# Kernel optimization log

Hardware: AMD Instinct MI355X
Metric: run time of the kernel (lower is better)

The kernel has to match this reference:

```python
import jax, jax.numpy as jnp
import numpy as np

T, J, D = 8192, 1024, 256  # context len, query len, 2*hidden


def setup_inputs() -> dict:
    key = jax.random.key(0)
    k1, k2, k3 = jax.random.split(key, 3)
    context = jax.random.normal(k1, (T, D), dtype=jnp.float32)
    query = jax.random.normal(k2, (J, D), dtype=jnp.float32)
    # sim_weight: Linear(3*D, 1, bias=False) -> single weight vector of length 3*D
    w = jax.random.normal(k3, (3 * D,), dtype=jnp.float32) * (1.0 / np.sqrt(3 * D))
    return {"context": context, "query": query, "w": w}


def reference(context, query, w):
    D = context.shape[1]
    # Decompose w.[c; q; c*q] into three rank-1 / matmul terms instead of
    # materializing [T,J,3D] concatenated pairs.
    w_c, w_q, w_m = w[:D], w[D:2 * D], w[2 * D:]
    # S[t,j] = c_t.w_c + q_j.w_q + (c_t * w_m).q_j   -> [T, J]
    S = (context @ w_c)[:, None] + (query @ w_q)[None, :] + (context * w_m) @ query.T
    # context-to-query attention: softmax over query positions j
    A = jax.nn.softmax(S, axis=1)                    # [T, J]
    context2query = A @ query                        # [T, D]
    # NOTE: original code takes b = max_j S (no softmax over t) and
    # h_tilde = sum_t b[t] * c_t  (a single [D] vector)
    b = jnp.max(S, axis=1)                           # [T]
    h_tilde = b @ context                            # [D]
    # G[t] = [c_t; c2q_t; c_t*c2q_t; c_t*h_tilde]    -> [T, 4D]
    G = jnp.concatenate(
        [context, context2query, context * context2query, context * h_tilde[None, :]],
        axis=1,
    )
    return G
```

## Files before the change

### kernel.cpp

```cpp
#include <hip/hip_runtime.h>
#include <stdint.h>

#define T_DIM 8192
#define J_DIM 1024
#define D_DIM 256

typedef __bf16 bf16x8 __attribute__((ext_vector_type(8)));
typedef float f32x4 __attribute__((ext_vector_type(4)));
typedef unsigned short u16x8 __attribute__((ext_vector_type(8)));
typedef unsigned short u16x4 __attribute__((ext_vector_type(4)));

__device__ inline unsigned short f2bf(float x) {
    unsigned u = __builtin_bit_cast(unsigned, x);
    u += 0x7FFFu + ((u >> 16) & 1u);
    return (unsigned short)(u >> 16);
}

__device__ inline void gll16(const void* g, void* l) {
    __builtin_amdgcn_global_load_lds(
        (const __attribute__((address_space(1))) unsigned int*)g,
        (__attribute__((address_space(3))) unsigned int*)l, 16, 0, 0);
}

__global__ __launch_bounds__(256) void prep_all(const float* __restrict__ ctx,
                                                const float* __restrict__ qry,
                                                const float* __restrict__ w,
                                                unsigned short* __restrict__ Cm,
                                                float* __restrict__ cw,
                                                unsigned short* __restrict__ Qb,
                                                unsigned short* __restrict__ QT,
                                                float* __restrict__ qw,
                                                float* __restrict__ stats) {
    int wid = threadIdx.x >> 6, lane = threadIdx.x & 63;
    if (blockIdx.x >= 2304) {
        int idx = (blockIdx.x - 2304) * 256 + threadIdx.x;
        if (idx < 2 * T_DIM + D_DIM) stats[idx] = 0.0f;
        return;
    }
    if (blockIdx.x < 2048) {
        int t = blockIdx.x * 4 + wid;
        float4 c  = *(const float4*)(ctx + (size_t)t * D_DIM + lane * 4);
        float4 wm = *(const float4*)(w + 2 * D_DIM + lane * 4);
        float4 wc = *(const float4*)(w + lane * 4);
        u16x4 cmv;
        cmv[0] = f2bf(c.x * wm.x);
        cmv[1] = f2bf(c.y * wm.y);
        cmv[2] = f2bf(c.z * wm.z);
        cmv[3] = f2bf(c.w * wm.w);
        *(u16x4*)(Cm + (size_t)t * D_DIM + lane * 4) = cmv;
        float s = c.x * wc.x + c.y * wc.y + c.z * wc.z + c.w * wc.w;
        #pragma unroll
        for (int o = 1; o < 64; o <<= 1) s += __shfl_xor(s, o);
        if (lane == 0) cw[t] = s;
    } else {
        int j = (blockIdx.x - 2048) * 4 + wid;
        float4 c  = *(const float4*)(qry + (size_t)j * D_DIM + lane * 4);
        float4 wq = *(const float4*)(w + D_DIM + lane * 4);
        u16x4 qv;
        qv[0] = f2bf(c.x);
        qv[1] = f2bf(c.y);
        qv[2] = f2bf(c.z);
        qv[3] = f2bf(c.w);
        *(u16x4*)(Qb + (size_t)j * D_DIM + lane * 4) = qv;
        int d0 = lane * 4;
        QT[(size_t)(d0 + 0) * J_DIM + j] = qv[0];
        QT[(size_t)(d0 + 1) * J_DIM + j] = qv[1];
        QT[(size_t)(d0 + 2) * J_DIM + j] = qv[2];
        QT[(size_t)(d0 + 3) * J_DIM + j] = qv[3];
        float s = c.x * wq.x + c.y * wq.y + c.z * wq.z + c.w * wq.w;
        #pragma unroll
        for (int o = 1; o < 64; o <<= 1) s += __shfl_xor(s, o);
        if (lane == 0) qw[j] = s;
    }
}

__global__ __launch_bounds__(256) void gemm_s(const unsigned short* __restrict__ Cm,
                                              const unsigned short* __restrict__ Qb,
                                              const float* __restrict__ qw,
                                              unsigned short* __restrict__ P,
                                              float* __restrict__ lsum,
                                              int* __restrict__ rmax) {
    __shared__ unsigned short SH[12288];
    __shared__ float statS[2][64];
    __shared__ float statM[2][64];
    unsigned short* As = SH;
    unsigned short* Bs = SH + 4096;
    int tid = threadIdx.x, lane = tid & 63, wv = tid >> 6;
    int wm = wv >> 1, wn = wv & 1;
    int bm = blockIdx.x & 127, bn = blockIdx.x >> 7;
    int cidx = lane & 15, rgrp = lane >> 4;
    int srow8 = lane >> 3;
    int swzc = (lane & 7) ^ srow8;
    f32x4 acc[2][4] = {};

    const unsigned short* Asrc = Cm + (size_t)(bm * 64 + srow8) * 256 + (swzc << 3);
    const unsigned short* Bsrc = Qb + (size_t)(bn * 128 + srow8) * 256 + (swzc << 3);

    for (int k0 = 0; k0 < 256; k0 += 64) {
        if (k0) __syncthreads();
        #pragma unroll
        for (int i = 0; i < 2; ++i) {
            int g = wv * 2 + i;
            gll16(Asrc + (size_t)(g * 8) * 256 + k0, As + g * 512);
        }
        #pragma unroll
        for (int i = 0; i < 4; ++i) {
            int g = wv * 4 + i;
            gll16(Bsrc + (size_t)(g * 8) * 256 + k0, Bs + g * 512);
        }
        __syncthreads();
        #pragma unroll
        for (int ks = 0; ks < 2; ++ks) {
            int klo = ks * 4 + rgrp;
            bf16x8 af[2], bfr[4];
            #pragma unroll
            for (int m = 0; m < 2; ++m) {
                int ra = wm * 32 + m * 16 + cidx;
                af[m] = __builtin_bit_cast(bf16x8,
                        *(const u16x8*)(As + ra * 64 + ((klo ^ (ra & 7)) << 3)));
            }
            #pragma unroll
            for (int n = 0; n < 4; ++n) {
                int rb = wn * 64 + n * 16 + cidx;
                bfr[n] = __builtin_bit_cast(bf16x8,
                        *(const u16x8*)(Bs + rb * 64 + ((klo ^ (rb & 7)) << 3)));
            }
            #pragma unroll
            for (int m = 0; m < 2; ++m)
                #pragma unroll
                for (int n = 0; n < 4; ++n)
                    acc[m][n] = __builtin_amdgcn_mfma_f32_16x16x32_bf16(af[m], bfr[n], acc[m][n], 0, 0, 0);
        }
    }

    float qwv[4];
    #pragma unroll
    for (int n = 0; n < 4; ++n) qwv[n] = qw[bn * 128 + wn * 64 + n * 16 + cidx];
    #pragma unroll
    for (int m = 0; m < 2; ++m) {
        #pragma unroll
        for (int rg = 0; rg < 4; ++rg) {
            float s = 0.f, mx = 0.f;
            #pragma unroll
            for (int n = 0; n < 4; ++n) {
                float p = __expf(acc[m][n][rg] + qwv[n]);
                acc[m][n][rg] = p;
                s += p;
                mx = fmaxf(mx, p);
            }
            #pragma unroll
            for (int o = 1; o < 16; o <<= 1) {
                s += __shfl_xor(s, o);
                mx = fmaxf(mx, __shfl_xor(mx, o));
            }
            if (cidx == 0) {
                int row = wm * 32 + m * 16 + rgrp * 4 + rg;
                statS[wn][row] = s;
                statM[wn][row] = mx;
            }
        }
    }
    __syncthreads();
    if (tid < 64) {
        atomicAdd(lsum + bm * 64 + tid, statS[0][tid] + statS[1][tid]);
        atomicMax(rmax + bm * 64 + tid,
                  __float_as_int(fmaxf(statM[0][tid], statM[1][tid])));
    }

    #pragma unroll
    for (int m = 0; m < 2; ++m)
        #pragma unroll
        for (int n = 0; n < 4; ++n)
            #pragma unroll
            for (int rg = 0; rg < 4; ++rg) {
                int row = wm * 32 + m * 16 + rgrp * 4 + rg;
                int col = wn * 64 + n * 16 + cidx;
                SH[row * 128 + (((col >> 3) ^ (row & 7)) << 3) + (col & 7)] = f2bf(acc[m][n][rg]);
            }
    __syncthreads();
    #pragma unroll
    for (int i = 0; i < 4; ++i) {
        int r = i * 16 + (tid >> 4);
        int c8 = tid & 15;
        u16x8 v = *(const u16x8*)(SH + r * 128 + ((c8 ^ (r & 7)) << 3));
        *(u16x8*)(P + (size_t)(bm * 64 + r) * J_DIM + bn * 128 + c8 * 8) = v;
    }
}

__global__ __launch_bounds__(256) void hb_kernel(const float* __restrict__ rmaxf,
                                                 const float* __restrict__ cw,
                                                 const float* __restrict__ ctx,
                                                 float* __restrict__ ht) {
    __shared__ float bsh[64];
    int tid = threadIdx.x;
    int t0b = blockIdx.x * 64;
    if (tid < 64) bsh[tid] = __logf(rmaxf[t0b + tid]) + cw[t0b + tid];
    __syncthreads();
    float pb = 0.f;
    #pragma unroll 8
    for (int r = 0; r < 64; ++r)
        pb += bsh[r] * ctx[(size_t)(t0b + r) * D_DIM + tid];
    atomicAdd(ht + tid, pb);
}

__global__ __launch_bounds__(256) void gemm_o(const unsigned short* __restrict__ P,
                                              const unsigned short* __restrict__ QT,
                                              const float* __restrict__ lsum,
                                              const float* __restrict__ ht,
                                              const float* __restrict__ ctx,
                                              float* __restrict__ G) {
    __shared__ unsigned short As[4096];
    __shared__ unsigned short Bs[4096];
    int tid = threadIdx.x, lane = tid & 63, wv = tid >> 6;
    int wm = wv >> 1, wn = wv & 1;
    int bm = blockIdx.x & 127, bn = blockIdx.x >> 7;
    int cidx = lane & 15, rgrp = lane >> 4;
    int srow8 = lane >> 3;
    int swzc = (lane & 7) ^ srow8;
    f32x4 acc[2][2] = {};

    const unsigned short* Ap = P  + (size_t)(bm * 64 + srow8) * J_DIM + (swzc << 3);
    const unsigned short* Bp = QT + (size_t)(bn * 64 + srow8) * J_DIM + (swzc << 3);

    for (int k0 = 0; k0 < 1024; k0 += 64) {
        if (k0) __syncthreads();
        #pragma unroll
        for (int i = 0; i < 2; ++i) {
            int g = wv * 2 + i;
            gll16(Ap + (size_t)(g * 8) * J_DIM + k0, As + g * 512);
        }
        #pragma unroll
        for (int i = 0; i < 2; ++i) {
            int g = wv * 2 + i;
            gll16(Bp + (size_t)(g * 8) * J_DIM + k0, Bs + g * 512);
        }
        __syncthreads();
        #pragma unroll
        for (int ks = 0; ks < 2; ++ks) {
            int klo = ks * 4 + rgrp;
            bf16x8 af[2], bfr[2];
            #pragma unroll
            for (int m = 0; m < 2; ++m) {
                int ra = wm * 32 + m * 16 + cidx;
                af[m] = __builtin_bit_cast(bf16x8,
                        *(const u16x8*)(As + ra * 64 + ((klo ^ (ra & 7)) << 3)));
            }
            #pragma unroll
            for (int n = 0; n < 2; ++n) {
                int rb = wn * 32 + n * 16 + cidx;
                bfr[n] = __builtin_bit_cast(bf16x8,
                        *(const u16x8*)(Bs + rb * 64 + ((klo ^ (rb & 7)) << 3)));
            }
            #pragma unroll
            for (int m = 0; m < 2; ++m)
                #pragma unroll
                for (int n = 0; n < 2; ++n)
                    acc[m][n] = __builtin_amdgcn_mfma_f32_16x16x32_bf16(af[m], bfr[n], acc[m][n], 0, 0, 0);
        }
    }

    float htv[2];
    #pragma unroll
    for (int n = 0; n < 2; ++n) htv[n] = ht[bn * 64 + wn * 32 + n * 16 + cidx];
    #pragma unroll
    for (int m = 0; m < 2; ++m) {
        #pragma unroll
        for (int rg = 0; rg < 4; ++rg) {
            int t = bm * 64 + wm * 32 + m * 16 + rgrp * 4 + rg;
            float linv = 1.0f / lsum[t];
            float* gr = G + (size_t)t * 1024;
            #pragma unroll
            for (int n = 0; n < 2; ++n) {
                int d = bn * 64 + wn * 32 + n * 16 + cidx;
                float val = acc[m][n][rg] * linv;
                float c = ctx[(size_t)t * D_DIM + d];
                gr[d]       = c;
                gr[256 + d] = val;
                gr[512 + d] = c * val;
                gr[768 + d] = c * htv[n];
            }
        }
    }
}

extern "C" void kernel_launch(void* const* d_in, const int* in_sizes, int n_in,
                              void* d_out, int out_size, void* d_ws, size_t ws_size,
                              hipStream_t stream) {
    (void)in_sizes; (void)n_in; (void)out_size; (void)ws_size;
    const float* ctx = (const float*)d_in[0];
    const float* qry = (const float*)d_in[1];
    const float* w   = (const float*)d_in[2];
    float* G = (float*)d_out;
    char* ws = (char*)d_ws;

    constexpr size_t OFF_P  = 0;
    constexpr size_t OFF_CM = OFF_P  + (size_t)T_DIM * J_DIM * 2;
    constexpr size_t OFF_QB = OFF_CM + (size_t)T_DIM * D_DIM * 2;
    constexpr size_t OFF_QT = OFF_QB + (size_t)J_DIM * D_DIM * 2;
    constexpr size_t OFF_CW = OFF_QT + (size_t)D_DIM * J_DIM * 2;
    constexpr size_t OFF_QW = OFF_CW + (size_t)T_DIM * 4;
    constexpr size_t OFF_ST = OFF_QW + (size_t)J_DIM * 4;

    unsigned short* P  = (unsigned short*)(ws + OFF_P);
    unsigned short* Cm = (unsigned short*)(ws + OFF_CM);
    unsigned short* Qb = (unsigned short*)(ws + OFF_QB);
    unsigned short* QT = (unsigned short*)(ws + OFF_QT);
    float* cw    = (float*)(ws + OFF_CW);
    float* qw    = (float*)(ws + OFF_QW);
    float* stats = (float*)(ws + OFF_ST);
    float* lsum  = stats;
    float* rmax  = stats + T_DIM;
    float* ht    = stats + 2 * T_DIM;

    prep_all<<<dim3(2369), 256, 0, stream>>>(ctx, qry, w, Cm, cw, Qb, QT, qw, stats);
    gemm_s<<<dim3(1024), 256, 0, stream>>>(Cm, Qb, qw, P, lsum, (int*)rmax);
    hb_kernel<<<dim3(128), 256, 0, stream>>>(rmax, cw, ctx, ht);
    gemm_o<<<dim3(512), 256, 0, stream>>>(P, QT, lsum, ht, ctx, G);
}
```

Measured before the change: 47.28 us.

## Double-buffer LDS tiles in both GEMM kernels to overlap loads with MFMA

Both GEMM kernels switch from a single LDS tile buffer to two buffers. The global-to-LDS load for the next K step is issued before computing on the current one, with an explicit vmcnt wait and barrier at the end of each step. This hides global load latency behind MFMA work and drops one barrier per iteration. The cost is doubled LDS use per block, which may lower occupancy, and gemm_s reuses the B buffer for its output staging.

```diff
diff --git a/kernel.cpp b/kernel.cpp
--- a/kernel.cpp
+++ b/kernel.cpp
@@ -20,6 +20,18 @@
     __builtin_amdgcn_global_load_lds(
         (const __attribute__((address_space(1))) unsigned int*)g,
         (__attribute__((address_space(3))) unsigned int*)l, 16, 0, 0);
+}
+
+__device__ inline void vm0_bar() {
+    asm volatile("s_waitcnt vmcnt(0)" ::: "memory");
+    __builtin_amdgcn_sched_barrier(0);
+    __builtin_amdgcn_s_barrier();
+    __builtin_amdgcn_sched_barrier(0);
+}
+__device__ inline void bar_only() {
+    __builtin_amdgcn_sched_barrier(0);
+    __builtin_amdgcn_s_barrier();
+    __builtin_amdgcn_sched_barrier(0);
 }
 
 __global__ __launch_bounds__(256) void prep_all(const float* __restrict__ ctx,
@@ -80,11 +92,10 @@
                                               unsigned short* __restrict__ P,
                                               float* __restrict__ lsum,
                                               int* __restrict__ rmax) {
-    __shared__ unsigned short SH[12288];
+    __shared__ unsigned short As[2][4096];
+    __shared__ unsigned short Bs[2][8192];
     __shared__ float statS[2][64];
     __shared__ float statM[2][64];
-    unsigned short* As = SH;
-    unsigned short* Bs = SH + 4096;
     int tid = threadIdx.x, lane = tid & 63, wv = tid >> 6;
     int wm = wv >> 1, wn = wv & 1;
     int bm = blockIdx.x & 127, bn = blockIdx.x >> 7;
@@ -96,19 +107,25 @@
     const unsigned short* Asrc = Cm + (size_t)(bm * 64 + srow8) * 256 + (swzc << 3);
     const unsigned short* Bsrc = Qb + (size_t)(bn * 128 + srow8) * 256 + (swzc << 3);
 
-    for (int k0 = 0; k0 < 256; k0 += 64) {
-        if (k0) __syncthreads();
+    auto stage = [&](int buf, int k0) {
         #pragma unroll
         for (int i = 0; i < 2; ++i) {
             int g = wv * 2 + i;
-            gll16(Asrc + (size_t)(g * 8) * 256 + k0, As + g * 512);
+            gll16(Asrc + (size_t)(g * 8) * 256 + k0, &As[buf][g * 512]);
         }
         #pragma unroll
         for (int i = 0; i < 4; ++i) {
             int g = wv * 4 + i;
-            gll16(Bsrc + (size_t)(g * 8) * 256 + k0, Bs + g * 512);
-        }
-        __syncthreads();
+            gll16(Bsrc + (size_t)(g * 8) * 256 + k0, &Bs[buf][g * 512]);
+        }
+    };
+
+    stage(0, 0);
+    vm0_bar();
+    #pragma unroll
+    for (int step = 0; step < 4; ++step) {
+        const int cur = step & 1;
+        if (step < 3) stage(cur ^ 1, (step + 1) * 64);
         #pragma unroll
         for (int ks = 0; ks < 2; ++ks) {
             int klo = ks * 4 + rgrp;
@@ -117,13 +134,13 @@
             for (int m = 0; m < 2; ++m) {
                 int ra = wm * 32 + m * 16 + cidx;
                 af[m] = __builtin_bit_cast(bf16x8,
-                        *(const u16x8*)(As + ra * 64 + ((klo ^ (ra & 7)) << 3)));
+                        *(const u16x8*)(&As[cur][ra * 64 + ((klo ^ (ra & 7)) << 3)]));
             }
             #pragma unroll
             for (int n = 0; n < 4; ++n) {
                 int rb = wn * 64 + n * 16 + cidx;
                 bfr[n] = __builtin_bit_cast(bf16x8,
-                        *(const u16x8*)(Bs + rb * 64 + ((klo ^ (rb & 7)) << 3)));
+                        *(const u16x8*)(&Bs[cur][rb * 64 + ((klo ^ (rb & 7)) << 3)]));
             }
             #pragma unroll
             for (int m = 0; m < 2; ++m)
@@ -131,6 +148,7 @@
                 for (int n = 0; n < 4; ++n)
                     acc[m][n] = __builtin_amdgcn_mfma_f32_16x16x32_bf16(af[m], bfr[n], acc[m][n], 0, 0, 0);
         }
+        if (step < 3) vm0_bar(); else bar_only();
     }
 
     float qwv[4];
@@ -167,6 +185,7 @@
                   __float_as_int(fmaxf(statM[0][tid], statM[1][tid])));
     }
 
+    unsigned short* PT = &Bs[0][0];
     #pragma unroll
     for (int m = 0; m < 2; ++m)
         #pragma unroll
@@ -175,14 +194,14 @@
             for (int rg = 0; rg < 4; ++rg) {
                 int row = wm * 32 + m * 16 + rgrp * 4 + rg;
                 int col = wn * 64 + n * 16 + cidx;
-                SH[row * 128 + (((col >> 3) ^ (row & 7)) << 3) + (col & 7)] = f2bf(acc[m][n][rg]);
+                PT[row * 128 + (((col >> 3) ^ (row & 7)) << 3) + (col & 7)] = f2bf(acc[m][n][rg]);
             }
     __syncthreads();
     #pragma unroll
     for (int i = 0; i < 4; ++i) {
         int r = i * 16 + (tid >> 4);
         int c8 = tid & 15;
-        u16x8 v = *(const u16x8*)(SH + r * 128 + ((c8 ^ (r & 7)) << 3));
+        u16x8 v = *(const u16x8*)(PT + r * 128 + ((c8 ^ (r & 7)) << 3));
         *(u16x8*)(P + (size_t)(bm * 64 + r) * J_DIM + bn * 128 + c8 * 8) = v;
     }
 }
@@ -209,8 +228,8 @@
                                               const float* __restrict__ ht,
                                               const float* __restrict__ ctx,
                                               float* __restrict__ G) {
-    __shared__ unsigned short As[4096];
-    __shared__ unsigned short Bs[4096];
+    __shared__ unsigned short As[2][4096];
+    __shared__ unsigned short Bs[2][4096];
     int tid = threadIdx.x, lane = tid & 63, wv = tid >> 6;
     int wm = wv >> 1, wn = wv & 1;
     int bm = blockIdx.x & 127, bn = blockIdx.x >> 7;
@@ -222,19 +241,21 @@
     const unsigned short* Ap = P  + (size_t)(bm * 64 + srow8) * J_DIM + (swzc << 3);
     const unsigned short* Bp = QT + (size_t)(bn * 64 + srow8) * J_DIM + (swzc << 3);
 
-    for (int k0 = 0; k0 < 1024; k0 += 64) {
-        if (k0) __syncthreads();
+    auto stage = [&](int buf, int k0) {
         #pragma unroll
         for (int i = 0; i < 2; ++i) {
             int g = wv * 2 + i;
-            gll16(Ap + (size_t)(g * 8) * J_DIM + k0, As + g * 512);
-        }
-        #pragma unroll
-        for (int i = 0; i < 2; ++i) {
-            int g = wv * 2 + i;
-            gll16(Bp + (size_t)(g * 8) * J_DIM + k0, Bs + g * 512);
-        }
-        __syncthreads();
+            gll16(Ap + (size_t)(g * 8) * J_DIM + k0, &As[buf][g * 512]);
+            gll16(Bp + (size_t)(g * 8) * J_DIM + k0, &Bs[buf][g * 512]);
+        }
+    };
+
+    stage(0, 0);
+    vm0_bar();
+    #pragma unroll
+    for (int step = 0; step < 16; ++step) {
+        const int cur = step & 1;
+        if (step < 15) stage(cur ^ 1, (step + 1) * 64);
         #pragma unroll
         for (int ks = 0; ks < 2; ++ks) {
             int klo = ks * 4 + rgrp;
@@ -243,13 +264,13 @@
             for (int m = 0; m < 2; ++m) {
                 int ra = wm * 32 + m * 16 + cidx;
                 af[m] = __builtin_bit_cast(bf16x8,
-                        *(const u16x8*)(As + ra * 64 + ((klo ^ (ra & 7)) << 3)));
+                        *(const u16x8*)(&As[cur][ra * 64 + ((klo ^ (ra & 7)) << 3)]));
             }
             #pragma unroll
             for (int n = 0; n < 2; ++n) {
                 int rb = wn * 32 + n * 16 + cidx;
                 bfr[n] = __builtin_bit_cast(bf16x8,
-                        *(const u16x8*)(Bs + rb * 64 + ((klo ^ (rb & 7)) << 3)));
+                        *(const u16x8*)(&Bs[cur][rb * 64 + ((klo ^ (rb & 7)) << 3)]));
             }
             #pragma unroll
             for (int m = 0; m < 2; ++m)
@@ -257,6 +278,7 @@
                 for (int n = 0; n < 2; ++n)
                     acc[m][n] = __builtin_amdgcn_mfma_f32_16x16x32_bf16(af[m], bfr[n], acc[m][n], 0, 0, 0);
         }
+        if (step < 15) vm0_bar(); else bar_only();
     }
 
     float htv[2];
```

Result: slower. 53.12 us (+12.4%).

## Enlarge gemm_s M tile to 128 rows and move c·w_c into hb_kernel

Applied to the files above, without the earlier changes.

The score GEMM now uses 128x128 tiles, giving each wave a 64x64 sub-tile instead of 32x64, which halves the grid to 512 blocks and raises reuse of the query tile loaded into LDS. The context-dot-w_c projection is no longer computed in the prep kernel and stored to workspace. hb_kernel now computes it directly from ctx, with four lanes per row. This removes the cw buffer and a shuffle reduction from prep, but adds register pressure (16 accumulators per wave) and fewer blocks for occupancy in gemm_s.

```diff
diff --git a/kernel.cpp b/kernel.cpp
--- a/kernel.cpp
+++ b/kernel.cpp
@@ -26,7 +26,6 @@
                                                 const float* __restrict__ qry,
                                                 const float* __restrict__ w,
                                                 unsigned short* __restrict__ Cm,
-                                                float* __restrict__ cw,
                                                 unsigned short* __restrict__ Qb,
                                                 unsigned short* __restrict__ QT,
                                                 float* __restrict__ qw,
@@ -41,17 +40,12 @@
         int t = blockIdx.x * 4 + wid;
         float4 c  = *(const float4*)(ctx + (size_t)t * D_DIM + lane * 4);
         float4 wm = *(const float4*)(w + 2 * D_DIM + lane * 4);
-        float4 wc = *(const float4*)(w + lane * 4);
         u16x4 cmv;
         cmv[0] = f2bf(c.x * wm.x);
         cmv[1] = f2bf(c.y * wm.y);
         cmv[2] = f2bf(c.z * wm.z);
         cmv[3] = f2bf(c.w * wm.w);
         *(u16x4*)(Cm + (size_t)t * D_DIM + lane * 4) = cmv;
-        float s = c.x * wc.x + c.y * wc.y + c.z * wc.z + c.w * wc.w;
-        #pragma unroll
-        for (int o = 1; o < 64; o <<= 1) s += __shfl_xor(s, o);
-        if (lane == 0) cw[t] = s;
     } else {
         int j = (blockIdx.x - 2048) * 4 + wid;
         float4 c  = *(const float4*)(qry + (size_t)j * D_DIM + lane * 4);
@@ -80,27 +74,27 @@
                                               unsigned short* __restrict__ P,
                                               float* __restrict__ lsum,
                                               int* __restrict__ rmax) {
-    __shared__ unsigned short SH[12288];
-    __shared__ float statS[2][64];
-    __shared__ float statM[2][64];
+    __shared__ unsigned short SH[16384];
+    __shared__ float statS[2][128];
+    __shared__ float statM[2][128];
     unsigned short* As = SH;
-    unsigned short* Bs = SH + 4096;
+    unsigned short* Bs = SH + 8192;
     int tid = threadIdx.x, lane = tid & 63, wv = tid >> 6;
     int wm = wv >> 1, wn = wv & 1;
-    int bm = blockIdx.x & 127, bn = blockIdx.x >> 7;
+    int bm = blockIdx.x & 63, bn = blockIdx.x >> 6;
     int cidx = lane & 15, rgrp = lane >> 4;
     int srow8 = lane >> 3;
     int swzc = (lane & 7) ^ srow8;
-    f32x4 acc[2][4] = {};
-
-    const unsigned short* Asrc = Cm + (size_t)(bm * 64 + srow8) * 256 + (swzc << 3);
+    f32x4 acc[4][4] = {};
+
+    const unsigned short* Asrc = Cm + (size_t)(bm * 128 + srow8) * 256 + (swzc << 3);
     const unsigned short* Bsrc = Qb + (size_t)(bn * 128 + srow8) * 256 + (swzc << 3);
 
     for (int k0 = 0; k0 < 256; k0 += 64) {
         if (k0) __syncthreads();
         #pragma unroll
-        for (int i = 0; i < 2; ++i) {
-            int g = wv * 2 + i;
+        for (int i = 0; i < 4; ++i) {
+            int g = wv * 4 + i;
             gll16(Asrc + (size_t)(g * 8) * 256 + k0, As + g * 512);
         }
         #pragma unroll
@@ -112,10 +106,10 @@
         #pragma unroll
         for (int ks = 0; ks < 2; ++ks) {
             int klo = ks * 4 + rgrp;
-            bf16x8 af[2], bfr[4];
-            #pragma unroll
-            for (int m = 0; m < 2; ++m) {
-                int ra = wm * 32 + m * 16 + cidx;
+            bf16x8 af[4], bfr[4];
+            #pragma unroll
+            for (int m = 0; m < 4; ++m) {
+                int ra = wm * 64 + m * 16 + cidx;
                 af[m] = __builtin_bit_cast(bf16x8,
                         *(const u16x8*)(As + ra * 64 + ((klo ^ (ra & 7)) << 3)));
             }
@@ -126,7 +120,7 @@
                         *(const u16x8*)(Bs + rb * 64 + ((klo ^ (rb & 7)) << 3)));
             }
             #pragma unroll
-            for (int m = 0; m < 2; ++m)
+            for (int m = 0; m < 4; ++m)
                 #pragma unroll
                 for (int n = 0; n < 4; ++n)
                     acc[m][n] = __builtin_amdgcn_mfma_f32_16x16x32_bf16(af[m], bfr[n], acc[m][n], 0, 0, 0);
@@ -137,7 +131,7 @@
     #pragma unroll
     for (int n = 0; n < 4; ++n) qwv[n] = qw[bn * 128 + wn * 64 + n * 16 + cidx];
     #pragma unroll
-    for (int m = 0; m < 2; ++m) {
+    for (int m = 0; m < 4; ++m) {
         #pragma unroll
         for (int rg = 0; rg < 4; ++rg) {
             float s = 0.f, mx = 0.f;
@@ -154,47 +148,61 @@
                 mx = fmaxf(mx, __shfl_xor(mx, o));
             }
             if (cidx == 0) {
-                int row = wm * 32 + m * 16 + rgrp * 4 + rg;
+                int row = wm * 64 + m * 16 + rgrp * 4 + rg;
                 statS[wn][row] = s;
                 statM[wn][row] = mx;
             }
         }
     }
     __syncthreads();
-    if (tid < 64) {
-        atomicAdd(lsum + bm * 64 + tid, statS[0][tid] + statS[1][tid]);
-        atomicMax(rmax + bm * 64 + tid,
+    if (tid < 128) {
+        atomicAdd(lsum + bm * 128 + tid, statS[0][tid] + statS[1][tid]);
+        atomicMax(rmax + bm * 128 + tid,
                   __float_as_int(fmaxf(statM[0][tid], statM[1][tid])));
     }
 
     #pragma unroll
-    for (int m = 0; m < 2; ++m)
+    for (int m = 0; m < 4; ++m)
         #pragma unroll
         for (int n = 0; n < 4; ++n)
             #pragma unroll
             for (int rg = 0; rg < 4; ++rg) {
-                int row = wm * 32 + m * 16 + rgrp * 4 + rg;
+                int row = wm * 64 + m * 16 + rgrp * 4 + rg;
                 int col = wn * 64 + n * 16 + cidx;
                 SH[row * 128 + (((col >> 3) ^ (row & 7)) << 3) + (col & 7)] = f2bf(acc[m][n][rg]);
             }
     __syncthreads();
     #pragma unroll
-    for (int i = 0; i < 4; ++i) {
+    for (int i = 0; i < 8; ++i) {
         int r = i * 16 + (tid >> 4);
         int c8 = tid & 15;
         u16x8 v = *(const u16x8*)(SH + r * 128 + ((c8 ^ (r & 7)) << 3));
-        *(u16x8*)(P + (size_t)(bm * 64 + r) * J_DIM + bn * 128 + c8 * 8) = v;
+        *(u16x8*)(P + (size_t)(bm * 128 + r) * J_DIM + bn * 128 + c8 * 8) = v;
     }
 }
 
 __global__ __launch_bounds__(256) void hb_kernel(const float* __restrict__ rmaxf,
-                                                 const float* __restrict__ cw,
+                                                 const float* __restrict__ w,
                                                  const float* __restrict__ ctx,
                                                  float* __restrict__ ht) {
     __shared__ float bsh[64];
     int tid = threadIdx.x;
     int t0b = blockIdx.x * 64;
-    if (tid < 64) bsh[tid] = __logf(rmaxf[t0b + tid]) + cw[t0b + tid];
+    int row = tid >> 2, q = tid & 3;
+    {
+        const float* cr = ctx + (size_t)(t0b + row) * D_DIM + q * 64;
+        const float* wc = w + q * 64;
+        float s = 0.f;
+        #pragma unroll
+        for (int i = 0; i < 16; ++i) {
+            float4 c = *(const float4*)(cr + i * 4);
+            float4 v = *(const float4*)(wc + i * 4);
+            s += c.x * v.x + c.y * v.y + c.z * v.z + c.w * v.w;
+        }
+        s += __shfl_xor(s, 1);
+        s += __shfl_xor(s, 2);
+        if (q == 0) bsh[row] = __logf(rmaxf[t0b + row]) + s;
+    }
     __syncthreads();
     float pb = 0.f;
     #pragma unroll 8
@@ -297,23 +305,21 @@
     constexpr size_t OFF_CM = OFF_P  + (size_t)T_DIM * J_DIM * 2;
     constexpr size_t OFF_QB = OFF_CM + (size_t)T_DIM * D_DIM * 2;
     constexpr size_t OFF_QT = OFF_QB + (size_t)J_DIM * D_DIM * 2;
-    constexpr size_t OFF_CW = OFF_QT + (size_t)D_DIM * J_DIM * 2;
-    constexpr size_t OFF_QW = OFF_CW + (size_t)T_DIM * 4;
+    constexpr size_t OFF_QW = OFF_QT + (size_t)D_DIM * J_DIM * 2;
     constexpr size_t OFF_ST = OFF_QW + (size_t)J_DIM * 4;
 
     unsigned short* P  = (unsigned short*)(ws + OFF_P);
     unsigned short* Cm = (unsigned short*)(ws + OFF_CM);
     unsigned short* Qb = (unsigned short*)(ws + OFF_QB);
     unsigned short* QT = (unsigned short*)(ws + OFF_QT);
-    float* cw    = (float*)(ws + OFF_CW);
     float* qw    = (float*)(ws + OFF_QW);
     float* stats = (float*)(ws + OFF_ST);
     float* lsum  = stats;
     float* rmax  = stats + T_DIM;
     float* ht    = stats + 2 * T_DIM;
 
-    prep_all<<<dim3(2369), 256, 0, stream>>>(ctx, qry, w, Cm, cw, Qb, QT, qw, stats);
-    gemm_s<<<dim3(1024), 256, 0, stream>>>(Cm, Qb, qw, P, lsum, (int*)rmax);
-    hb_kernel<<<dim3(128), 256, 0, stream>>>(rmax, cw, ctx, ht);
+    prep_all<<<dim3(2369), 256, 0, stream>>>(ctx, qry, w, Cm, Qb, QT, qw, stats);
+    gemm_s<<<dim3(512), 256, 0, stream>>>(Cm, Qb, qw, P, lsum, (int*)rmax);
+    hb_kernel<<<dim3(128), 256, 0, stream>>>(rmax, w, ctx, ht);
     gemm_o<<<dim3(512), 256, 0, stream>>>(P, QT, lsum, ht, ctx, G);
 }
```

After: 52.22 us. 1.1x slower.
